# Kernel optimization log

Hardware: AMD Instinct MI355X
Metric: run time of the kernel (lower is better)

Reference implementation:

```python
import jax, jax.numpy as jnp
import numpy as np

NUM_CLASSES = 1000
K_PROTOS = 5
FEAT_DIM = 1024
BATCH = 16384


def _l2norm(x, axis=-1, eps=1e-12):
    # matches torch.nn.functional.normalize
    n = jnp.linalg.norm(x, axis=axis, keepdims=True)
    return x / jnp.maximum(n, eps)


def setup_inputs() -> dict:
    key = jax.random.key(0)
    k1, k2, k3 = jax.random.split(key, 3)
    z = jax.random.normal(k1, (BATCH, FEAT_DIM), dtype=jnp.float32)
    y = jax.random.randint(k2, (BATCH,), 0, NUM_CLASSES, dtype=jnp.int64)
    # learned prototype bank, dense [C, K, D] (all slots populated)
    P = jax.random.normal(k3, (NUM_CLASSES, K_PROTOS, FEAT_DIM), dtype=jnp.float32)
    return {"z": z, "y": y, "P": P}


def reference(z, y, P):
    """Returns (pos_sim [B], neg_sim [B]): max cosine sim to same-class and
    other-class prototypes respectively (PrototypeBank.forward)."""
    C, K, D = P.shape
    z_n = _l2norm(z)                     # [B, D]
    P_n = _l2norm(P).reshape(C * K, D)   # [C*K, D]
    sim = jnp.einsum('bd,pd->bp', z_n, P_n)  # [B, C*K]
    proto_labels = jnp.repeat(jnp.arange(C, dtype=y.dtype), K)  # [C*K]
    same = proto_labels[None, :] == y[:, None]  # [B, C*K]
    neg_inf = jnp.asarray(-jnp.inf, sim.dtype)
    pos_sim = jnp.max(jnp.where(same, sim, neg_inf), axis=1)
    neg_sim = jnp.max(jnp.where(same, neg_inf, sim), axis=1)
    return pos_sim, neg_sim
```

## Files before the change

### kernel.cpp

```cpp
#include <hip/hip_runtime.h>
#include <hip/hip_bf16.h>
#include <stdint.h>

#define BATCH 16384
#define D 1024
#define NCLS 1000
#define NPROTO 5000
#define NPROTO_PAD 5120
#define BM 64
#define NCH 5
#define NKT 32
#define KSTRIDE (320 * 64 * 8)

typedef float f32x4 __attribute__((ext_vector_type(4)));
typedef __bf16 bf16x8 __attribute__((ext_vector_type(8)));

__device__ __forceinline__ unsigned short f2bf(float x) {
    unsigned u = __float_as_uint(x);
    u += 0x7FFFu + ((u >> 16) & 1u);
    return (unsigned short)(u >> 16);
}

__global__ __launch_bounds__(256) void k_prep(
        const float* __restrict__ z, const float* __restrict__ P,
        unsigned short* __restrict__ zb, unsigned short* __restrict__ pbf) {
    const int b = blockIdx.x;
    const int t = threadIdx.x;
    const int e0 = 4 * t;
    const float* src = nullptr;
    unsigned short* dst;
    if (b < BATCH) {
        src = z + (size_t)b * D;
        dst = zb + (size_t)b * D + e0;
    } else {
        const int r = b - BATCH;
        const int kt = e0 >> 5;
        const int lk = (e0 >> 3) & 3;
        const int ke = e0 & 7;
        dst = pbf + (((size_t)kt * 320 + (r >> 4)) * 64 + (r & 15) + 16 * lk) * 8 + ke;
        if (r < NPROTO) src = P + (size_t)r * D;
    }
    if (src == nullptr) {
        *(ushort4*)dst = make_ushort4(0, 0, 0, 0);
        return;
    }
    float4 v = ((const float4*)src)[t];
    float ss = v.x * v.x + v.y * v.y + v.z * v.z + v.w * v.w;
    #pragma unroll
    for (int o = 32; o >= 1; o >>= 1) ss += __shfl_xor(ss, o);
    __shared__ float red[4];
    const int wave = t >> 6;
    if ((t & 63) == 0) red[wave] = ss;
    __syncthreads();
    const float s = red[0] + red[1] + red[2] + red[3];
    const float inv = 1.0f / fmaxf(sqrtf(s), 1e-12f);
    ushort4 o4;
    o4.x = f2bf(v.x * inv); o4.y = f2bf(v.y * inv);
    o4.z = f2bf(v.z * inv); o4.w = f2bf(v.w * inv);
    *(ushort4*)dst = o4;
}

#define MM(A, B, C) __builtin_amdgcn_mfma_f32_16x16x32_bf16(A, B, C, 0, 0, 0)

__global__ __launch_bounds__(1024, 4) void k_gemm(
        const unsigned short* __restrict__ zb,
        const unsigned short* __restrict__ pbf,
        const int* __restrict__ y,
        float* __restrict__ out) {
    __shared__ __align__(16) unsigned short LA[NKT][4][64][8];
    __shared__ float redP[16][64];
    __shared__ float redN[16][64];

    const int t = threadIdx.x;
    const int w = t >> 6;
    const int lane = t & 63;
    const int lm = lane & 15, lk = lane >> 4;
    const int rowbase = blockIdx.x * BM;

    {
        const int ktw = lane >> 1;
        const int lk0 = (lane & 1) * 2;
        #pragma unroll
        for (int j = 0; j < 4; ++j) {
            const int r = w * 4 + j;
            const unsigned short* gp = zb + (size_t)(rowbase + r) * D + lane * 16;
            const bf16x8 v0 = *(const bf16x8*)gp;
            const bf16x8 v1 = *(const bf16x8*)(gp + 8);
            *(bf16x8*)&LA[ktw][r >> 4][(r & 15) + 16 * lk0][0] = v0;
            *(bf16x8*)&LA[ktw][r >> 4][(r & 15) + 16 * (lk0 + 1)][0] = v1;
        }
    }
    int yv[16];
    #pragma unroll
    for (int mi = 0; mi < 4; ++mi)
        #pragma unroll
        for (int r = 0; r < 4; ++r)
            yv[mi * 4 + r] = y[rowbase + mi * 16 + lk * 4 + r];

    __syncthreads();

    float pmv[16], nmv[16];
    #pragma unroll
    for (int i = 0; i < 16; ++i) { pmv[i] = -INFINITY; nmv[i] = -INFINITY; }

    #pragma unroll 1
    for (int c = 0; c < NCH; ++c) {
        const int grp0 = c * 64 + w * 4;
        const unsigned short* pB = pbf + ((size_t)grp0 * 64 + lane) * 8;

        f32x4 acc[4][4];
        #pragma unroll
        for (int mi = 0; mi < 4; ++mi)
            #pragma unroll
            for (int ni = 0; ni < 4; ++ni) {
                f32x4 z4 = {0.0f, 0.0f, 0.0f, 0.0f};
                acc[mi][ni] = z4;
            }

        bf16x8 bc0 = *(const bf16x8*)(pB);
        bf16x8 bc1 = *(const bf16x8*)(pB + 512);
        bf16x8 bc2 = *(const bf16x8*)(pB + 1024);
        bf16x8 bc3 = *(const bf16x8*)(pB + 1536);
        bf16x8 bn0, bn1, bn2, bn3;

        #pragma unroll 1
        for (int kt = 0; kt < NKT; kt += 2) {
            {
                const unsigned short* q = pB + (size_t)(kt + 1) * KSTRIDE;
                bn0 = *(const bf16x8*)(q);
                bn1 = *(const bf16x8*)(q + 512);
                bn2 = *(const bf16x8*)(q + 1024);
                bn3 = *(const bf16x8*)(q + 1536);
            }
            {
                const bf16x8 a0 = *(const bf16x8*)&LA[kt][0][lane][0];
                const bf16x8 a1 = *(const bf16x8*)&LA[kt][1][lane][0];
                const bf16x8 a2 = *(const bf16x8*)&LA[kt][2][lane][0];
                const bf16x8 a3 = *(const bf16x8*)&LA[kt][3][lane][0];
                acc[0][0] = MM(a0, bc0, acc[0][0]);
                acc[0][1] = MM(a0, bc1, acc[0][1]);
                acc[0][2] = MM(a0, bc2, acc[0][2]);
                acc[0][3] = MM(a0, bc3, acc[0][3]);
                acc[1][0] = MM(a1, bc0, acc[1][0]);
                acc[1][1] = MM(a1, bc1, acc[1][1]);
                acc[1][2] = MM(a1, bc2, acc[1][2]);
                acc[1][3] = MM(a1, bc3, acc[1][3]);
                acc[2][0] = MM(a2, bc0, acc[2][0]);
                acc[2][1] = MM(a2, bc1, acc[2][1]);
                acc[2][2] = MM(a2, bc2, acc[2][2]);
                acc[2][3] = MM(a2, bc3, acc[2][3]);
                acc[3][0] = MM(a3, bc0, acc[3][0]);
                acc[3][1] = MM(a3, bc1, acc[3][1]);
                acc[3][2] = MM(a3, bc2, acc[3][2]);
                acc[3][3] = MM(a3, bc3, acc[3][3]);
            }
            {
                const int ktn = (kt + 2 < NKT) ? kt + 2 : NKT - 1;
                const unsigned short* q = pB + (size_t)ktn * KSTRIDE;
                bc0 = *(const bf16x8*)(q);
                bc1 = *(const bf16x8*)(q + 512);
                bc2 = *(const bf16x8*)(q + 1024);
                bc3 = *(const bf16x8*)(q + 1536);
            }
            {
                const bf16x8 a0 = *(const bf16x8*)&LA[kt + 1][0][lane][0];
                const bf16x8 a1 = *(const bf16x8*)&LA[kt + 1][1][lane][0];
                const bf16x8 a2 = *(const bf16x8*)&LA[kt + 1][2][lane][0];
                const bf16x8 a3 = *(const bf16x8*)&LA[kt + 1][3][lane][0];
                acc[0][0] = MM(a0, bn0, acc[0][0]);
                acc[0][1] = MM(a0, bn1, acc[0][1]);
                acc[0][2] = MM(a0, bn2, acc[0][2]);
                acc[0][3] = MM(a0, bn3, acc[0][3]);
                acc[1][0] = MM(a1, bn0, acc[1][0]);
                acc[1][1] = MM(a1, bn1, acc[1][1]);
                acc[1][2] = MM(a1, bn2, acc[1][2]);
                acc[1][3] = MM(a1, bn3, acc[1][3]);
                acc[2][0] = MM(a2, bn0, acc[2][0]);
                acc[2][1] = MM(a2, bn1, acc[2][1]);
                acc[2][2] = MM(a2, bn2, acc[2][2]);
                acc[2][3] = MM(a2, bn3, acc[2][3]);
                acc[3][0] = MM(a3, bn0, acc[3][0]);
                acc[3][1] = MM(a3, bn1, acc[3][1]);
                acc[3][2] = MM(a3, bn2, acc[3][2]);
                acc[3][3] = MM(a3, bn3, acc[3][3]);
            }
        }

        #pragma unroll
        for (int ni = 0; ni < 4; ++ni) {
            const unsigned col = (unsigned)(c * 1024 + w * 64 + ni * 16 + lm);
            const unsigned lbl = __umulhi(col, 0xCCCCCCCDu) >> 2;
            const bool valid = col < NPROTO;
            #pragma unroll
            for (int mi = 0; mi < 4; ++mi)
                #pragma unroll
                for (int r = 0; r < 4; ++r) {
                    const float v = acc[mi][ni][r];
                    const bool same = (lbl == (unsigned)yv[mi * 4 + r]);
                    const int i = mi * 4 + r;
                    pmv[i] = same ? fmaxf(pmv[i], v) : pmv[i];
                    nmv[i] = (!same && valid) ? fmaxf(nmv[i], v) : nmv[i];
                }
        }
    }

    #pragma unroll
    for (int i = 0; i < 16; ++i) {
        #pragma unroll
        for (int off = 1; off < 16; off <<= 1) {
            pmv[i] = fmaxf(pmv[i], __shfl_xor(pmv[i], off));
            nmv[i] = fmaxf(nmv[i], __shfl_xor(nmv[i], off));
        }
    }
    if (lm == 0) {
        #pragma unroll
        for (int mi = 0; mi < 4; ++mi)
            #pragma unroll
            for (int r = 0; r < 4; ++r) {
                redP[w][mi * 16 + lk * 4 + r] = pmv[mi * 4 + r];
                redN[w][mi * 16 + lk * 4 + r] = nmv[mi * 4 + r];
            }
    }
    __syncthreads();
    if (t < 64) {
        float p = redP[0][t], n = redN[0][t];
        #pragma unroll
        for (int ww = 1; ww < 16; ++ww) {
            p = fmaxf(p, redP[ww][t]);
            n = fmaxf(n, redN[ww][t]);
        }
        out[rowbase + t] = p;
        out[BATCH + rowbase + t] = n;
    }
}

extern "C" void kernel_launch(void* const* d_in, const int* in_sizes, int n_in,
                              void* d_out, int out_size, void* d_ws, size_t ws_size,
                              hipStream_t stream) {
    const float* z = (const float*)d_in[0];
    const int*   y = (const int*)d_in[1];
    const float* P = (const float*)d_in[2];

    unsigned short* zb = (unsigned short*)d_ws;
    unsigned short* pbf = zb + (size_t)BATCH * D;
    float* out = (float*)d_out;

    k_prep<<<BATCH + NPROTO_PAD, 256, 0, stream>>>(z, P, zb, pbf);
    k_gemm<<<BATCH / BM, 1024, 0, stream>>>(zb, pbf, y, out);
}
```

Baseline: 180.9 us.

## Shrink per-wave N tile to 3 groups, reduce epilogue per chunk, add setprio

Each wave now covers 3 prototype groups of 16 columns per chunk instead of 4, with 7 chunks over a padded bank of 5376 prototypes. The per-row running max registers and label registers are removed. Instead, each chunk does the shuffle reduction and folds into shared-memory partials, which lowers VGPR pressure. MFMA blocks are wrapped in s_setprio so waves can overlap compute with loads. The cost is more padded wasted columns, a smaller MFMA tile per B load, and more frequent shuffle and LDS reduction work.

After: 190.7 us. +5.4%, slower.

```diff
diff --git a/kernel.cpp b/kernel.cpp
--- a/kernel.cpp
+++ b/kernel.cpp
@@ -6,11 +6,12 @@
 #define D 1024
 #define NCLS 1000
 #define NPROTO 5000
-#define NPROTO_PAD 5120
+#define NPROTO_PAD 5376
+#define NGRP 336
 #define BM 64
-#define NCH 5
+#define NCH 7
 #define NKT 32
-#define KSTRIDE (320 * 64 * 8)
+#define KSTRIDE (NGRP * 64 * 8)
 
 typedef float f32x4 __attribute__((ext_vector_type(4)));
 typedef __bf16 bf16x8 __attribute__((ext_vector_type(8)));
@@ -37,7 +38,7 @@
         const int kt = e0 >> 5;
         const int lk = (e0 >> 3) & 3;
         const int ke = e0 & 7;
-        dst = pbf + (((size_t)kt * 320 + (r >> 4)) * 64 + (r & 15) + 16 * lk) * 8 + ke;
+        dst = pbf + (((size_t)kt * NGRP + (r >> 4)) * 64 + (r & 15) + 16 * lk) * 8 + ke;
         if (r < NPROTO) src = P + (size_t)r * D;
     }
     if (src == nullptr) {
@@ -77,6 +78,9 @@
     const int lm = lane & 15, lk = lane >> 4;
     const int rowbase = blockIdx.x * BM;
 
+    redP[t >> 6][t & 63] = -INFINITY;
+    redN[t >> 6][t & 63] = -INFINITY;
+
     {
         const int ktw = lane >> 1;
         const int lk0 = (lane & 1) * 2;
@@ -90,29 +94,18 @@
             *(bf16x8*)&LA[ktw][r >> 4][(r & 15) + 16 * (lk0 + 1)][0] = v1;
         }
     }
-    int yv[16];
-    #pragma unroll
-    for (int mi = 0; mi < 4; ++mi)
-        #pragma unroll
-        for (int r = 0; r < 4; ++r)
-            yv[mi * 4 + r] = y[rowbase + mi * 16 + lk * 4 + r];
-
     __syncthreads();
-
-    float pmv[16], nmv[16];
-    #pragma unroll
-    for (int i = 0; i < 16; ++i) { pmv[i] = -INFINITY; nmv[i] = -INFINITY; }
 
     #pragma unroll 1
     for (int c = 0; c < NCH; ++c) {
-        const int grp0 = c * 64 + w * 4;
+        const int grp0 = c * 48 + w * 3;
         const unsigned short* pB = pbf + ((size_t)grp0 * 64 + lane) * 8;
 
-        f32x4 acc[4][4];
+        f32x4 acc[4][3];
         #pragma unroll
         for (int mi = 0; mi < 4; ++mi)
             #pragma unroll
-            for (int ni = 0; ni < 4; ++ni) {
+            for (int ni = 0; ni < 3; ++ni) {
                 f32x4 z4 = {0.0f, 0.0f, 0.0f, 0.0f};
                 acc[mi][ni] = z4;
             }
@@ -120,8 +113,7 @@
         bf16x8 bc0 = *(const bf16x8*)(pB);
         bf16x8 bc1 = *(const bf16x8*)(pB + 512);
         bf16x8 bc2 = *(const bf16x8*)(pB + 1024);
-        bf16x8 bc3 = *(const bf16x8*)(pB + 1536);
-        bf16x8 bn0, bn1, bn2, bn3;
+        bf16x8 bn0, bn1, bn2;
 
         #pragma unroll 1
         for (int kt = 0; kt < NKT; kt += 2) {
@@ -130,29 +122,26 @@
                 bn0 = *(const bf16x8*)(q);
                 bn1 = *(const bf16x8*)(q + 512);
                 bn2 = *(const bf16x8*)(q + 1024);
-                bn3 = *(const bf16x8*)(q + 1536);
             }
             {
                 const bf16x8 a0 = *(const bf16x8*)&LA[kt][0][lane][0];
                 const bf16x8 a1 = *(const bf16x8*)&LA[kt][1][lane][0];
                 const bf16x8 a2 = *(const bf16x8*)&LA[kt][2][lane][0];
                 const bf16x8 a3 = *(const bf16x8*)&LA[kt][3][lane][0];
+                __builtin_amdgcn_s_setprio(1);
                 acc[0][0] = MM(a0, bc0, acc[0][0]);
                 acc[0][1] = MM(a0, bc1, acc[0][1]);
                 acc[0][2] = MM(a0, bc2, acc[0][2]);
-                acc[0][3] = MM(a0, bc3, acc[0][3]);
                 acc[1][0] = MM(a1, bc0, acc[1][0]);
                 acc[1][1] = MM(a1, bc1, acc[1][1]);
                 acc[1][2] = MM(a1, bc2, acc[1][2]);
-                acc[1][3] = MM(a1, bc3, acc[1][3]);
                 acc[2][0] = MM(a2, bc0, acc[2][0]);
                 acc[2][1] = MM(a2, bc1, acc[2][1]);
                 acc[2][2] = MM(a2, bc2, acc[2][2]);
-                acc[2][3] = MM(a2, bc3, acc[2][3]);
                 acc[3][0] = MM(a3, bc0, acc[3][0]);
                 acc[3][1] = MM(a3, bc1, acc[3][1]);
                 acc[3][2] = MM(a3, bc2, acc[3][2]);
-                acc[3][3] = MM(a3, bc3, acc[3][3]);
+                __builtin_amdgcn_s_setprio(0);
             }
             {
                 const int ktn = (kt + 2 < NKT) ? kt + 2 : NKT - 1;
@@ -160,67 +149,58 @@
                 bc0 = *(const bf16x8*)(q);
                 bc1 = *(const bf16x8*)(q + 512);
                 bc2 = *(const bf16x8*)(q + 1024);
-                bc3 = *(const bf16x8*)(q + 1536);
             }
             {
                 const bf16x8 a0 = *(const bf16x8*)&LA[kt + 1][0][lane][0];
                 const bf16x8 a1 = *(const bf16x8*)&LA[kt + 1][1][lane][0];
                 const bf16x8 a2 = *(const bf16x8*)&LA[kt + 1][2][lane][0];
                 const bf16x8 a3 = *(const bf16x8*)&LA[kt + 1][3][lane][0];
+                __builtin_amdgcn_s_setprio(1);
                 acc[0][0] = MM(a0, bn0, acc[0][0]);
                 acc[0][1] = MM(a0, bn1, acc[0][1]);
                 acc[0][2] = MM(a0, bn2, acc[0][2]);
-                acc[0][3] = MM(a0, bn3, acc[0][3]);
                 acc[1][0] = MM(a1, bn0, acc[1][0]);
                 acc[1][1] = MM(a1, bn1, acc[1][1]);
                 acc[1][2] = MM(a1, bn2, acc[1][2]);
-                acc[1][3] = MM(a1, bn3, acc[1][3]);
                 acc[2][0] = MM(a2, bn0, acc[2][0]);
                 acc[2][1] = MM(a2, bn1, acc[2][1]);
                 acc[2][2] = MM(a2, bn2, acc[2][2]);
-                acc[2][3] = MM(a2, bn3, acc[2][3]);
                 acc[3][0] = MM(a3, bn0, acc[3][0]);
                 acc[3][1] = MM(a3, bn1, acc[3][1]);
                 acc[3][2] = MM(a3, bn2, acc[3][2]);
-                acc[3][3] = MM(a3, bn3, acc[3][3]);
-            }
-        }
-
-        #pragma unroll
-        for (int ni = 0; ni < 4; ++ni) {
-            const unsigned col = (unsigned)(c * 1024 + w * 64 + ni * 16 + lm);
-            const unsigned lbl = __umulhi(col, 0xCCCCCCCDu) >> 2;
-            const bool valid = col < NPROTO;
-            #pragma unroll
-            for (int mi = 0; mi < 4; ++mi)
-                #pragma unroll
-                for (int r = 0; r < 4; ++r) {
-                    const float v = acc[mi][ni][r];
-                    const bool same = (lbl == (unsigned)yv[mi * 4 + r]);
-                    const int i = mi * 4 + r;
-                    pmv[i] = same ? fmaxf(pmv[i], v) : pmv[i];
-                    nmv[i] = (!same && valid) ? fmaxf(nmv[i], v) : nmv[i];
-                }
-        }
-    }
-
-    #pragma unroll
-    for (int i = 0; i < 16; ++i) {
-        #pragma unroll
-        for (int off = 1; off < 16; off <<= 1) {
-            pmv[i] = fmaxf(pmv[i], __shfl_xor(pmv[i], off));
-            nmv[i] = fmaxf(nmv[i], __shfl_xor(nmv[i], off));
-        }
-    }
-    if (lm == 0) {
-        #pragma unroll
-        for (int mi = 0; mi < 4; ++mi)
+                __builtin_amdgcn_s_setprio(0);
+            }
+        }
+
+        #pragma unroll
+        for (int mi = 0; mi < 4; ++mi) {
             #pragma unroll
             for (int r = 0; r < 4; ++r) {
-                redP[w][mi * 16 + lk * 4 + r] = pmv[mi * 4 + r];
-                redN[w][mi * 16 + lk * 4 + r] = nmv[mi * 4 + r];
-            }
-    }
+                const int row = mi * 16 + lk * 4 + r;
+                const unsigned yv = (unsigned)y[rowbase + row];
+                float pm = -INFINITY, nm = -INFINITY;
+                #pragma unroll
+                for (int ni = 0; ni < 3; ++ni) {
+                    const unsigned col = (unsigned)(c * 768 + w * 48 + ni * 16 + lm);
+                    const unsigned lbl = __umulhi(col, 0xCCCCCCCDu) >> 2;
+                    const float v = acc[mi][ni][r];
+                    const bool same = (lbl == yv);
+                    pm = same ? fmaxf(pm, v) : pm;
+                    nm = (!same && col < NPROTO) ? fmaxf(nm, v) : nm;
+                }
+                #pragma unroll
+                for (int off = 1; off < 16; off <<= 1) {
+                    pm = fmaxf(pm, __shfl_xor(pm, off));
+                    nm = fmaxf(nm, __shfl_xor(nm, off));
+                }
+                if (lm == 0) {
+                    redP[w][row] = fmaxf(redP[w][row], pm);
+                    redN[w][row] = fmaxf(redN[w][row], nm);
+                }
+            }
+        }
+    }
+
     __syncthreads();
     if (t < 64) {
         float p = redP[0][t], n = redN[0][t];
```
